# Optimization experiments

Hardware: AMD Instinct MI355X
Metric: run time of the kernel (lower is better)

## Reference

```python
import jax, jax.numpy as jnp
import numpy as np

B, S, H, NH = 1, 2048, 4096, 32
HD = H // NH
INV_NORM = 1.0 / float(np.sqrt(HD))
BETA = 1.0
NEG_MIN = float(np.finfo(np.float32).min)


def setup_inputs() -> dict:
    key = jax.random.key(0)
    ks = jax.random.split(key, 8)
    hidden_states = jax.random.normal(ks[0], (B, S, H), dtype=jnp.float32)
    residual = jax.random.normal(ks[1], (B, S, H), dtype=jnp.float32)
    # ALiBi: per-head slope * position, shape [B*NH, 1, S] as HF BLOOM builds it
    slopes = jnp.asarray(2.0 ** (-8.0 * (np.arange(1, NH + 1) / NH)), dtype=jnp.float32)
    pos = jnp.arange(S, dtype=jnp.float32)
    alibi = (slopes[:, None, None] * pos[None, None, :])  # [NH,1,S]
    alibi = jnp.tile(alibi, (B, 1, 1))  # [B*NH,1,S]
    # causal mask: True where attention is NOT allowed
    attention_mask = jnp.triu(jnp.ones((S, S), dtype=bool), k=1)[None, None]  # [1,1,S,S]
    w_qkv = jax.random.normal(ks[2], (3 * H, H), dtype=jnp.float32) * 0.02
    b_qkv = jax.random.normal(ks[3], (3 * H,), dtype=jnp.float32) * 0.02
    w_dense = jax.random.normal(ks[4], (H, H), dtype=jnp.float32) * 0.02
    b_dense = jax.random.normal(ks[5], (H,), dtype=jnp.float32) * 0.02
    return {
        'hidden_states': hidden_states, 'residual': residual, 'alibi': alibi,
        'attention_mask': attention_mask, 'w_qkv': w_qkv, 'b_qkv': b_qkv,
        'w_dense': w_dense, 'b_dense': b_dense,
    }


def reference(hidden_states, residual, alibi, attention_mask, w_qkv, b_qkv, w_dense, b_dense):
    # fused QKV projection, interleaved per-head split as in BLOOM
    fused = hidden_states @ w_qkv.T + b_qkv  # [B,S,3H]
    fused = fused.reshape(B, S, NH, 3, HD)
    q, k, v = fused[..., 0, :], fused[..., 1, :], fused[..., 2, :]  # [B,S,NH,HD]
    # baddbmm: beta*alibi + alpha * Q K^T
    scores = jnp.einsum('bqhd,bkhd->bhqk', q, k) * INV_NORM  # [B,NH,S,S]
    scores = scores + BETA * alibi.reshape(B, NH, 1, S)
    scores = jnp.where(attention_mask, NEG_MIN, scores)
    probs = jax.nn.softmax(scores, axis=-1)  # fp32 softmax (inputs already fp32)
    ctx = jnp.einsum('bhqk,bkhd->bqhd', probs, v).reshape(B, S, H)
    out = ctx @ w_dense.T + b_dense
    return out + residual  # dropout_add with p=0 in eval
```

## Files before the change

### kernel.cpp

```cpp
#include <hip/hip_runtime.h>
#include <cstdint>
#include <cstddef>

#define S_LEN 2048
#define H_DIM 4096
#define NHEAD 32
#define HD    128
#define N_QKV 12288
#define INV_NORM 0.08838834764831845f

typedef __bf16 bf16_t;
typedef bf16_t bf16x8 __attribute__((ext_vector_type(8)));
typedef bf16_t bf16x4 __attribute__((ext_vector_type(4)));
typedef float  f32x4  __attribute__((ext_vector_type(4)));

static_assert(sizeof(bf16x8) == 16, "bf16x8 must be 16B");

__device__ __forceinline__ f32x4 mfma16(bf16x8 a, bf16x8 b, f32x4 c) {
  return __builtin_amdgcn_mfma_f32_16x16x32_bf16(a, b, c, 0, 0, 0);
}

typedef __attribute__((address_space(1))) void gas_void;
typedef __attribute__((address_space(3))) void las_void;
__device__ __forceinline__ void async16(const void* g, void* l) {
  __builtin_amdgcn_global_load_lds((const gas_void*)g,
                                   (las_void*)(uint32_t)(uintptr_t)l,
                                   16, 0, 0);
}

#define SWZ(x)    ((x) ^ ((((x) >> 7) & 7) << 4))
#define SWZ256(x) ((x) ^ ((((x) >> 8) & 7) << 4))
#define VMCNT(n) asm volatile("s_waitcnt vmcnt(" #n ")" ::: "memory")
#define LGKM0()  asm volatile("s_waitcnt lgkmcnt(0)" ::: "memory")
#define SCHED0() __builtin_amdgcn_sched_barrier(0)
#define BARRIER() __builtin_amdgcn_s_barrier()

typedef float f32v4 __attribute__((ext_vector_type(4)));
#define NX4 ((S_LEN * H_DIM) / 4)
#define NQ4 ((N_QKV * H_DIM) / 4)
#define ND4 ((H_DIM * H_DIM) / 4)
__global__ void cvt_all(const float* __restrict__ x, const float* __restrict__ wq,
                        const float* __restrict__ wd,
                        bf16_t* __restrict__ xb, bf16_t* __restrict__ wqb,
                        bf16_t* __restrict__ wdb) {
  int i = blockIdx.x * 256 + threadIdx.x;
  const float* src; bf16_t* dst; int j;
  if (i < NX4) { src = x; dst = xb; j = i; }
  else if (i < NX4 + NQ4) { src = wq; dst = wqb; j = i - NX4; }
  else if (i < NX4 + NQ4 + ND4) { src = wd; dst = wdb; j = i - NX4 - NQ4; }
  else return;
  f32v4 v = ((const f32v4*)src)[j];
  bf16x4 r;
  r[0] = (bf16_t)v[0]; r[1] = (bf16_t)v[1]; r[2] = (bf16_t)v[2]; r[3] = (bf16_t)v[3];
  ((bf16x4*)dst)[j] = r;
}

template <int MODE, int BN>
__global__ __launch_bounds__(512, 2)
void gemm_pipe(const bf16_t* __restrict__ Ag,
               const bf16_t* __restrict__ Bg,
               const float* __restrict__ bias,
               const float* __restrict__ residual,
               bf16_t* __restrict__ q_out,
               bf16_t* __restrict__ k_out,
               bf16_t* __restrict__ v_out,
               float* __restrict__ f_out,
               int ncol)
{
  constexpr int NFRAG = BN / 32;
  constexpr int NBU   = BN / 64;
  constexpr int BBUF  = BN * 128;
  __shared__ __align__(16) char sm[65536 + 2 * BBUF];
  char* smA = sm;
  char* smB = sm + 65536;
  const int Kdim = H_DIM;
  const int NT = Kdim >> 6;

  const int tid = threadIdx.x, lane = tid & 63, w = tid >> 6;
  const int wm = w >> 1, wn = w & 1;
  const int lo = lane & 15, g = lane >> 4;

  const int nwg = gridDim.x * gridDim.y;
  const int bid = blockIdx.y * gridDim.x + blockIdx.x;
  const int cpx = nwg >> 3;
  const int sbid = (bid & 7) * cpx + (bid >> 3);
  const int brow = (sbid / ncol) << 8;
  const int bcol = (sbid % ncol) * BN;

  auto stageA = [&](int t, int u) {
    const int lin = u * 8192 + w * 1024 + lane * 16;
    const int lg = SWZ(lin);
    const bf16_t* src = Ag + (size_t)(brow + (lg >> 7)) * Kdim + (t << 6) + ((lg & 127) >> 1);
    async16(src, smA + ((t & 1) * 32768 + u * 8192 + w * 1024));
  };
  auto stageB = [&](int t, int u) {
    const int lin = u * 8192 + w * 1024 + lane * 16;
    const int lg = SWZ(lin);
    const bf16_t* src = Bg + (size_t)(bcol + (lg >> 7)) * Kdim + (t << 6) + ((lg & 127) >> 1);
    async16(src, smB + ((t & 1) * BBUF + u * 8192 + w * 1024));
  };
  auto rdA = [&](int t, int mi, int ks) -> bf16x8 {
    const int lin = (wm * 64 + mi * 16 + lo) * 128 + ks * 64 + g * 16;
    return *(const bf16x8*)(smA + (t & 1) * 32768 + SWZ(lin));
  };
  auto rdB = [&](int t, int ni, int ks) -> bf16x8 {
    const int lin = (wn * (BN / 2) + ni * 16 + lo) * 128 + ks * 64 + g * 16;
    return *(const bf16x8*)(smB + (t & 1) * BBUF + SWZ(lin));
  };

  f32x4 acc[4][NFRAG] = {};
  bf16x8 bfrag[NFRAG][2];

#pragma unroll
  for (int u = 0; u < NBU; ++u) stageB(0, u);
  stageA(0, 0); stageA(0, 1); stageA(0, 2); stageA(0, 3);
#pragma unroll
  for (int u = 0; u < NBU; ++u) stageB(1, u);
  if constexpr (NBU == 3) { VMCNT(3); } else { VMCNT(2); }
  SCHED0();
  BARRIER();

  for (int t = 0; t < NT; ++t) {
#pragma unroll
    for (int half = 0; half < 2; ++half) {
      bf16x8 afrag[2][2];
      if (half == 0) {
#pragma unroll
        for (int ni = 0; ni < NFRAG; ++ni)
#pragma unroll
          for (int ks = 0; ks < 2; ++ks)
            bfrag[ni][ks] = rdB(t, ni, ks);
      }
#pragma unroll
      for (int j = 0; j < 2; ++j)
#pragma unroll
        for (int ks = 0; ks < 2; ++ks)
          afrag[j][ks] = rdA(t, half * 2 + j, ks);

      if (half == 0) {
        if (t + 1 < NT) { stageA(t + 1, 0); stageA(t + 1, 1); stageA(t + 1, 2); stageA(t + 1, 3); }
      } else {
        if (t + 2 < NT) {
#pragma unroll
          for (int u = 0; u < NBU; ++u) stageB(t + 2, u);
        }
      }

      SCHED0();
      BARRIER();
      if (half == 1) {
        if (t < NT - 2) {
          if constexpr (NBU == 3) { VMCNT(3); } else { VMCNT(2); }
        } else if (t == NT - 2) {
          VMCNT(0);
        }
      }
      LGKM0();
      SCHED0();
      __builtin_amdgcn_s_setprio(1);
#pragma unroll
      for (int j = 0; j < 2; ++j)
#pragma unroll
        for (int ni = 0; ni < NFRAG; ++ni)
#pragma unroll
          for (int ks = 0; ks < 2; ++ks)
            acc[half * 2 + j][ni] = mfma16(afrag[j][ks], bfrag[ni][ks], acc[half * 2 + j][ni]);
      __builtin_amdgcn_s_setprio(0);
      SCHED0();
      BARRIER();
    }
  }

  if (MODE == 0) {
#pragma unroll
    for (int ni = 0; ni < NFRAG; ++ni) {
      const int cg = bcol + wn * (BN / 2) + ni * 16 + lo;
      const int chunk = cg >> 7;
      const int slot = chunk % 3, head = chunk / 3;
      bf16_t* dst = (slot == 0) ? q_out : (slot == 1) ? k_out : v_out;
      dst += (size_t)head * S_LEN * HD;
      const float scale = (slot == 0) ? INV_NORM : 1.0f;
      const float bb = bias[cg];
      const int d = cg & 127;
#pragma unroll
      for (int mi = 0; mi < 4; ++mi) {
#pragma unroll
        for (int jj = 0; jj < 4; ++jj) {
          const int r = brow + wm * 64 + mi * 16 + g * 4 + jj;
          dst[(size_t)r * HD + d] = (bf16_t)((acc[mi][ni][jj] + bb) * scale);
        }
      }
    }
  } else {
#pragma unroll
    for (int ni = 0; ni < NFRAG; ++ni) {
      const int cg = bcol + wn * (BN / 2) + ni * 16 + lo;
      const float bb = bias[cg];
#pragma unroll
      for (int mi = 0; mi < 4; ++mi) {
#pragma unroll
        for (int jj = 0; jj < 4; ++jj) {
          const int r = brow + wm * 64 + mi * 16 + g * 4 + jj;
          f_out[(size_t)r * H_DIM + cg] = acc[mi][ni][jj] + bb + residual[(size_t)r * H_DIM + cg];
        }
      }
    }
  }
}

__global__ __launch_bounds__(256, 2)
void attn_kernel(const bf16_t* __restrict__ Qg,
                 const bf16_t* __restrict__ Kg,
                 const bf16_t* __restrict__ Vg,
                 const float* __restrict__ alibi,
                 bf16_t* __restrict__ ctx)
{
  const int bid = blockIdx.x;
  const int h  = (bid & 7) * 4 + ((bid >> 3) & 3);
  const int qb = 31 - (bid >> 5);
  const int tid = threadIdx.x, lane = tid & 63, w = tid >> 6;
  const int lo = lane & 15, g = lane >> 4;

  __shared__ __align__(16) bf16_t Ks[2][64 * 128];
  __shared__ bf16_t Vt[2][128][72];
  __shared__ bf16_t Pl[4][16][72];

  const bf16_t* Qh = Qg + ((size_t)h * S_LEN + qb * 64 + w * 16) * HD;
  const bf16_t* Kh = Kg + (size_t)h * S_LEN * HD;
  const bf16_t* Vh = Vg + (size_t)h * S_LEN * HD;
  const float slope = alibi[(size_t)h * S_LEN + 1];

  bf16x8 qf[4];
#pragma unroll
  for (int ds = 0; ds < 4; ds++)
    qf[ds] = *(const bf16x8*)(Qh + lo * HD + ds * 32 + g * 8);

  f32x4 oacc[8] = {};
  float m_r[4], l_r[4];
#pragma unroll
  for (int jj = 0; jj < 4; jj++) { m_r[jj] = -INFINITY; l_r[jj] = 0.f; }

  const int ntiles = qb + 1;
  const int q_base = qb * 64 + w * 16;

  bf16x8 vvA[4], vvB[4];
#pragma unroll
  for (int u = 0; u < 4; ++u)
    vvA[u] = *(const bf16x8*)(Vh + (size_t)lane * HD + (u * 4 + w) * 8);
#pragma unroll
  for (int u = 0; u < 4; ++u) {
    const int lin = u * 4096 + tid * 16;
    const int lg = SWZ256(lin);
    async16(Kh + (size_t)(lg >> 8) * HD + ((lg & 255) >> 1),
            (char*)&Ks[0][0] + u * 4096 + w * 1024);
  }

  for (int kt = 0; kt < ntiles; ++kt) {
    const int k0 = kt * 64;
    const int cur = kt & 1;
    const bf16x8* vvC = cur ? vvB : vvA;
    bf16x8* vvN = cur ? vvA : vvB;

#pragma unroll
    for (int u = 0; u < 4; ++u) {
      const int d0 = (u * 4 + w) * 8;
#pragma unroll
      for (int e = 0; e < 8; ++e) Vt[cur][d0 + e][lane] = vvC[u][e];
    }
    if (kt + 1 < ntiles) {
      const bf16_t* Vn = Vh + (size_t)(k0 + 64) * HD;
#pragma unroll
      for (int u = 0; u < 4; ++u)
        vvN[u] = *(const bf16x8*)(Vn + (size_t)lane * HD + (u * 4 + w) * 8);
    }
    SCHED0();
    if (kt + 1 < ntiles) { VMCNT(4); } else { VMCNT(0); }
    LGKM0();
    SCHED0();
    BARRIER();
    SCHED0();
    if (kt + 1 < ntiles) {
      const bf16_t* Kn = Kh + (size_t)(k0 + 64) * HD;
#pragma unroll
      for (int u = 0; u < 4; ++u) {
        const int lin = u * 4096 + tid * 16;
        const int lg = SWZ256(lin);
        async16(Kn + (size_t)(lg >> 8) * HD + ((lg & 255) >> 1),
                (char*)&Ks[cur ^ 1][0] + u * 4096 + w * 1024);
      }
    }

    f32x4 sacc[4] = {};
#pragma unroll
    for (int kc = 0; kc < 4; ++kc) {
      bf16x8 kf[4];
#pragma unroll
      for (int ds = 0; ds < 4; ++ds) {
        const int lin = (kc * 16 + lo) * 256 + ds * 64 + g * 16;
        kf[ds] = *(const bf16x8*)((const char*)&Ks[cur][0] + SWZ256(lin));
      }
      __builtin_amdgcn_s_setprio(1);
#pragma unroll
      for (int ds = 0; ds < 4; ++ds)
        sacc[kc] = mfma16(qf[ds], kf[ds], sacc[kc]);
      __builtin_amdgcn_s_setprio(0);
    }

    float sv[4][4];
#pragma unroll
    for (int kc = 0; kc < 4; kc++) {
      const float alk = slope * (float)(k0 + kc * 16 + lo);
#pragma unroll
      for (int jj = 0; jj < 4; jj++)
        sv[kc][jj] = sacc[kc][jj] + alk;
    }
    if (kt == ntiles - 1) {
#pragma unroll
      for (int kc = 0; kc < 4; kc++) {
        const int k_gl = k0 + kc * 16 + lo;
#pragma unroll
        for (int jj = 0; jj < 4; jj++) {
          const int q_gl = q_base + g * 4 + jj;
          if (k_gl > q_gl) sv[kc][jj] = -INFINITY;
        }
      }
    }

#pragma unroll
    for (int jj = 0; jj < 4; jj++) {
      float mx = fmaxf(fmaxf(sv[0][jj], sv[1][jj]), fmaxf(sv[2][jj], sv[3][jj]));
      mx = fmaxf(mx, __shfl_xor(mx, 1, 64));
      mx = fmaxf(mx, __shfl_xor(mx, 2, 64));
      mx = fmaxf(mx, __shfl_xor(mx, 4, 64));
      mx = fmaxf(mx, __shfl_xor(mx, 8, 64));
      const float mn = fmaxf(m_r[jj], mx);
      const float sc = __expf(m_r[jj] - mn);
      m_r[jj] = mn;
      l_r[jj] *= sc;
#pragma unroll
      for (int df = 0; df < 8; df++) oacc[df][jj] *= sc;
      float rs = 0.f;
#pragma unroll
      for (int kc = 0; kc < 4; kc++) {
        const float p = __expf(sv[kc][jj] - mn);
        rs += p;
        Pl[w][g * 4 + jj][kc * 16 + lo] = (bf16_t)p;
      }
      rs += __shfl_xor(rs, 1, 64);
      rs += __shfl_xor(rs, 2, 64);
      rs += __shfl_xor(rs, 4, 64);
      rs += __shfl_xor(rs, 8, 64);
      l_r[jj] += rs;
    }

#pragma unroll
    for (int ks = 0; ks < 2; ++ks) {
      bf16x8 pa = *(const bf16x8*)&Pl[w][lo][ks * 32 + g * 8];
#pragma unroll
      for (int df = 0; df < 8; df++) {
        bf16x8 vf = *(const bf16x8*)&Vt[cur][df * 16 + lo][ks * 32 + g * 8];
        __builtin_amdgcn_s_setprio(1);
        oacc[df] = mfma16(pa, vf, oacc[df]);
        __builtin_amdgcn_s_setprio(0);
      }
    }
  }

#pragma unroll
  for (int jj = 0; jj < 4; jj++) {
    const float inv = 1.0f / l_r[jj];
    const int r = q_base + g * 4 + jj;
#pragma unroll
    for (int df = 0; df < 8; df++) {
      const int d = df * 16 + lo;
      ctx[(size_t)r * H_DIM + h * HD + d] = (bf16_t)(oacc[df][jj] * inv);
    }
  }
}

extern "C" void kernel_launch(void* const* d_in, const int* in_sizes, int n_in,
                              void* d_out, int out_size, void* d_ws, size_t ws_size,
                              hipStream_t stream) {
  const float* hidden   = (const float*)d_in[0];
  const float* residual = (const float*)d_in[1];
  const float* alibi    = (const float*)d_in[2];
  const float* w_qkv    = (const float*)d_in[4];
  const float* b_qkv    = (const float*)d_in[5];
  const float* w_dense  = (const float*)d_in[6];
  const float* b_dense  = (const float*)d_in[7];
  float* out = (float*)d_out;

  char* ws = (char*)d_ws;
  bf16_t* Xb  = (bf16_t*)(ws);
  bf16_t* Wqb = (bf16_t*)(ws + 16777216);
  bf16_t* Wdb = (bf16_t*)(ws + 117440512);
  bf16_t* Qb  = (bf16_t*)(ws + 150994944);
  bf16_t* Kb  = (bf16_t*)(ws + 167772160);
  bf16_t* Vb  = (bf16_t*)(ws + 184549376);
  bf16_t* Ctx = (bf16_t*)(ws + 201326592);

  {
    int n4 = NX4 + NQ4 + ND4;
    cvt_all<<<(n4 + 255) / 256, 256, 0, stream>>>(hidden, w_qkv, w_dense, Xb, Wqb, Wdb);
  }

  gemm_pipe<0, 192><<<dim3(N_QKV / 192, S_LEN / 256), 512, 0, stream>>>(
      Xb, Wqb, b_qkv, nullptr, Qb, Kb, Vb, nullptr, N_QKV / 192);

  attn_kernel<<<NHEAD * (S_LEN / 64), 256, 0, stream>>>(Qb, Kb, Vb, alibi, Ctx);

  gemm_pipe<1, 128><<<dim3(H_DIM / 128, S_LEN / 256), 512, 0, stream>>>(
      Ctx, Wdb, b_dense, residual, nullptr, nullptr, nullptr, out, H_DIM / 128);
}
```

Before: 458.6 us.

## Load GEMM A operand directly from global into registers, dropping LDS staging

The A tile is no longer staged through shared memory. Each wave loads its A fragments straight from global memory into double-buffered registers one k-tile ahead, and only B goes through LDS with async copies. This cuts LDS footprint and LDS read traffic for A and changes the vmcnt accounting to cover the per-thread register loads. In exchange it raises register pressure, and the global loads are less coalesced (16B per lane across rows), so load latency may be exposed.

Result: slower. 685.6 us (+49.5%).

```diff
diff --git a/kernel.cpp b/kernel.cpp
--- a/kernel.cpp
+++ b/kernel.cpp
@@ -70,9 +70,7 @@
   constexpr int NFRAG = BN / 32;
   constexpr int NBU   = BN / 64;
   constexpr int BBUF  = BN * 128;
-  __shared__ __align__(16) char sm[65536 + 2 * BBUF];
-  char* smA = sm;
-  char* smB = sm + 65536;
+  __shared__ __align__(16) char smB[2 * BBUF];
   const int Kdim = H_DIM;
   const int NT = Kdim >> 6;
 
@@ -87,88 +85,92 @@
   const int brow = (sbid / ncol) << 8;
   const int bcol = (sbid % ncol) * BN;
 
-  auto stageA = [&](int t, int u) {
-    const int lin = u * 8192 + w * 1024 + lane * 16;
-    const int lg = SWZ(lin);
-    const bf16_t* src = Ag + (size_t)(brow + (lg >> 7)) * Kdim + (t << 6) + ((lg & 127) >> 1);
-    async16(src, smA + ((t & 1) * 32768 + u * 8192 + w * 1024));
-  };
   auto stageB = [&](int t, int u) {
     const int lin = u * 8192 + w * 1024 + lane * 16;
     const int lg = SWZ(lin);
     const bf16_t* src = Bg + (size_t)(bcol + (lg >> 7)) * Kdim + (t << 6) + ((lg & 127) >> 1);
     async16(src, smB + ((t & 1) * BBUF + u * 8192 + w * 1024));
   };
-  auto rdA = [&](int t, int mi, int ks) -> bf16x8 {
-    const int lin = (wm * 64 + mi * 16 + lo) * 128 + ks * 64 + g * 16;
-    return *(const bf16x8*)(smA + (t & 1) * 32768 + SWZ(lin));
-  };
   auto rdB = [&](int t, int ni, int ks) -> bf16x8 {
     const int lin = (wn * (BN / 2) + ni * 16 + lo) * 128 + ks * 64 + g * 16;
     return *(const bf16x8*)(smB + (t & 1) * BBUF + SWZ(lin));
   };
 
+  const bf16_t* Arow = Ag + (size_t)(brow + wm * 64 + lo) * Kdim + g * 8;
+  auto loadA = [&](bf16x8 (&rr)[4][2], int t) {
+#pragma unroll
+    for (int mi = 0; mi < 4; ++mi)
+#pragma unroll
+      for (int ks = 0; ks < 2; ++ks)
+        rr[mi][ks] = *(const bf16x8*)(Arow + (size_t)mi * 16 * Kdim + t * 64 + ks * 32);
+  };
+
   f32x4 acc[4][NFRAG] = {};
   bf16x8 bfrag[NFRAG][2];
+  bf16x8 rAa[4][2], rAb[4][2];
 
 #pragma unroll
   for (int u = 0; u < NBU; ++u) stageB(0, u);
-  stageA(0, 0); stageA(0, 1); stageA(0, 2); stageA(0, 3);
+  SCHED0();
+  loadA(rAa, 0);
+  SCHED0();
 #pragma unroll
   for (int u = 0; u < NBU; ++u) stageB(1, u);
-  if constexpr (NBU == 3) { VMCNT(3); } else { VMCNT(2); }
+  if constexpr (NBU == 3) { VMCNT(11); } else { VMCNT(10); }
   SCHED0();
   BARRIER();
 
-  for (int t = 0; t < NT; ++t) {
-#pragma unroll
-    for (int half = 0; half < 2; ++half) {
-      bf16x8 afrag[2][2];
-      if (half == 0) {
-#pragma unroll
-        for (int ni = 0; ni < NFRAG; ++ni)
-#pragma unroll
-          for (int ks = 0; ks < 2; ++ks)
-            bfrag[ni][ks] = rdB(t, ni, ks);
-      }
-#pragma unroll
-      for (int j = 0; j < 2; ++j)
+  auto ktile = [&](int t, bf16x8 (&rUse)[4][2], bf16x8 (&rNext)[4][2]) {
+#pragma unroll
+    for (int ni = 0; ni < NFRAG; ++ni)
+#pragma unroll
+      for (int ks = 0; ks < 2; ++ks)
+        bfrag[ni][ks] = rdB(t, ni, ks);
+    SCHED0();
+    if (t + 1 < NT) loadA(rNext, t + 1);
+    SCHED0();
+    BARRIER();
+    LGKM0();
+    SCHED0();
+    __builtin_amdgcn_s_setprio(1);
+#pragma unroll
+    for (int j = 0; j < 2; ++j)
+#pragma unroll
+      for (int ni = 0; ni < NFRAG; ++ni)
 #pragma unroll
         for (int ks = 0; ks < 2; ++ks)
-          afrag[j][ks] = rdA(t, half * 2 + j, ks);
-
-      if (half == 0) {
-        if (t + 1 < NT) { stageA(t + 1, 0); stageA(t + 1, 1); stageA(t + 1, 2); stageA(t + 1, 3); }
-      } else {
-        if (t + 2 < NT) {
-#pragma unroll
-          for (int u = 0; u < NBU; ++u) stageB(t + 2, u);
-        }
-      }
-
-      SCHED0();
-      BARRIER();
-      if (half == 1) {
-        if (t < NT - 2) {
-          if constexpr (NBU == 3) { VMCNT(3); } else { VMCNT(2); }
-        } else if (t == NT - 2) {
-          VMCNT(0);
-        }
-      }
-      LGKM0();
-      SCHED0();
-      __builtin_amdgcn_s_setprio(1);
-#pragma unroll
-      for (int j = 0; j < 2; ++j)
-#pragma unroll
-        for (int ni = 0; ni < NFRAG; ++ni)
-#pragma unroll
-          for (int ks = 0; ks < 2; ++ks)
-            acc[half * 2 + j][ni] = mfma16(afrag[j][ks], bfrag[ni][ks], acc[half * 2 + j][ni]);
-      __builtin_amdgcn_s_setprio(0);
-      SCHED0();
-      BARRIER();
-    }
+          acc[j][ni] = mfma16(rUse[j][ks], bfrag[ni][ks], acc[j][ni]);
+    __builtin_amdgcn_s_setprio(0);
+    SCHED0();
+    BARRIER();
+    if (t + 2 < NT) {
+#pragma unroll
+      for (int u = 0; u < NBU; ++u) stageB(t + 2, u);
+    }
+    SCHED0();
+    BARRIER();
+    if (t < NT - 2) {
+      if constexpr (NBU == 3) { VMCNT(11); } else { VMCNT(10); }
+    } else if (t == NT - 2) {
+      VMCNT(8);
+    }
+    SCHED0();
+    __builtin_amdgcn_s_setprio(1);
+#pragma unroll
+    for (int j = 2; j < 4; ++j)
+#pragma unroll
+      for (int ni = 0; ni < NFRAG; ++ni)
+#pragma unroll
+        for (int ks = 0; ks < 2; ++ks)
+          acc[j][ni] = mfma16(rUse[j][ks], bfrag[ni][ks], acc[j][ni]);
+    __builtin_amdgcn_s_setprio(0);
+    SCHED0();
+    BARRIER();
+  };
+
+  for (int tt = 0; tt < NT; tt += 2) {
+    ktile(tt,     rAa, rAb);
+    ktile(tt + 1, rAb, rAa);
   }
 
   if (MODE == 0) {
```
